# Kernel optimization log

Measured on AMD Instinct MI355X. Metric: run time of the kernel, lower is better.

## Reference

```python
import jax, jax.numpy as jnp
from jax import lax
import numpy as np

B, T, D = 8, 512, 512
TS = 2 * T          # skip length = upsampled length
DI, DS, DTR, K, NL = 2 * D, 16, 32, 4, 2  # d_inner, d_state, dt_rank, d_conv, n_layers


def setup_inputs() -> dict:
    key = jax.random.key(0)
    ks = jax.random.split(key, 12)
    f = lambda k, s: jax.random.normal(k, s, dtype=jnp.float32)
    sc = 0.02
    A_log = jnp.log(jnp.arange(1, DS + 1, dtype=jnp.float32))  # S4D-real init
    A_log = jnp.tile(A_log[None, None, :], (NL, DI, 1))
    return {
        "x": f(ks[0], (B, T, D)),
        "skip": f(ks[1], (B, TS, D)),
        "up_w": f(ks[2], (D, D, K)) * sc,        # torch ConvTranspose1d weight (in,out,k)
        "up_b": jnp.zeros((D,), jnp.float32),
        "merge_w": f(ks[3], (D, 2 * D)) * sc,    # 1x1 conv (out,in)
        "merge_b": jnp.zeros((D,), jnp.float32),
        "ln_w": jnp.ones((D,), jnp.float32),
        "ln_b": jnp.zeros((D,), jnp.float32),
        "in_proj_w": f(ks[4], (NL, 2 * DI, D)) * sc,
        "conv_w": f(ks[5], (NL, DI, K)) * sc,    # depthwise causal conv
        "conv_b": jnp.zeros((NL, DI), jnp.float32),
        "x_proj_w": f(ks[6], (NL, DTR + 2 * DS, DI)) * sc,
        "dt_proj_w": f(ks[7], (NL, DI, DTR)) * sc,
        "dt_proj_b": f(ks[8], (NL, DI)) * 0.1,
        "A_log": A_log,
        "D_param": jnp.ones((NL, DI), jnp.float32),
        "out_proj_w": f(ks[9], (NL, D, DI)) * sc,
    }


def _mamba(u, iw, cw, cb, xw, dw, db, alog, dpar, ow):
    # u: (B,L,D) -> (B,L,D). Standard Mamba block (expand=2, d_state=16, d_conv=4).
    b, L, _ = u.shape
    di, ds, dtr = cw.shape[0], alog.shape[1], dw.shape[1]
    xz = jnp.einsum('bld,ed->ble', u, iw)          # (B,L,2*di)
    xi, z = jnp.split(xz, 2, axis=-1)
    # depthwise causal conv over time
    xc = lax.conv_general_dilated(xi.transpose(0, 2, 1), cw[:, None, :], (1,),
                                  [(K - 1, 0)], feature_group_count=di,
                                  dimension_numbers=('NCH', 'OIH', 'NCH')) + cb[:, None]
    xc = jax.nn.silu(xc).transpose(0, 2, 1)        # (B,L,di)
    xdbl = jnp.einsum('bld,ed->ble', xc, xw)       # (B,L,dtr+2*ds)
    dt, Bm, Cm = jnp.split(xdbl, [dtr, dtr + ds], axis=-1)
    dt = jax.nn.softplus(jnp.einsum('blr,dr->bld', dt, dw) + db)  # (B,L,di)
    A = -jnp.exp(alog)                              # (di,ds)

    def step(h, inp):
        dt_t, B_t, C_t, u_t = inp                   # (B,di),(B,ds),(B,ds),(B,di)
        h = jnp.exp(dt_t[:, :, None] * A) * h + (dt_t * u_t)[:, :, None] * B_t[:, None, :]
        return h, jnp.einsum('bds,bs->bd', h, C_t)

    h0 = jnp.zeros((b, di, ds), u.dtype)
    _, ys = lax.scan(step, h0, (dt.transpose(1, 0, 2), Bm.transpose(1, 0, 2),
                                Cm.transpose(1, 0, 2), xc.transpose(1, 0, 2)))
    y = ys.transpose(1, 0, 2) + dpar * xc           # D skip connection
    y = y * jax.nn.silu(z)                          # gating
    return jnp.einsum('bld,od->blo', y, ow)


def reference(x, skip, up_w, up_b, merge_w, merge_b, ln_w, ln_b,
              in_proj_w, conv_w, conv_b, x_proj_w, dt_proj_w, dt_proj_b,
              A_log, D_param, out_proj_w):
    # ConvTranspose1d(k=4,s=2,p=1): dilated conv with flipped, transposed kernel
    kern = jnp.flip(jnp.swapaxes(up_w, 0, 1), -1)   # (out,in,k)
    xu = lax.conv_general_dilated(x.transpose(0, 2, 1), kern, (1,), [(2, 2)],
                                  lhs_dilation=(2,),
                                  dimension_numbers=('NCH', 'OIH', 'NCH')) + up_b[:, None]
    Ts = skip.shape[1]
    xu = xu[:, :, :Ts]                              # T_up == T_skip here (2T)
    cat = jnp.concatenate([xu.transpose(0, 2, 1), skip], axis=-1)  # (B,Ts,2D)
    merged = jnp.einsum('btc,oc->bto', cat, merge_w) + merge_b     # 1x1 conv merge
    mu = merged.mean(-1, keepdims=True)
    var = merged.var(-1, keepdims=True)
    out = (merged - mu) * lax.rsqrt(var + 1e-5) * ln_w + ln_b      # LayerNorm
    for i in range(in_proj_w.shape[0]):             # stacked Mamba layers
        out = _mamba(out, in_proj_w[i], conv_w[i], conv_b[i], x_proj_w[i],
                     dt_proj_w[i], dt_proj_b[i], A_log[i], D_param[i], out_proj_w[i])
    return out
```

## Files before the change

### kernel.cpp

```cpp
#include <hip/hip_runtime.h>

#define DEV __device__ __forceinline__

typedef short  bf16x8 __attribute__((ext_vector_type(8)));
typedef float  f32x4  __attribute__((ext_vector_type(4)));

DEV unsigned short f2b(float f) {
    unsigned int u = __float_as_uint(f);
    u += 0x7fffu + ((u >> 16) & 1u);
    return (unsigned short)(u >> 16);
}
DEV float b2f(unsigned short h) { return __uint_as_float((unsigned int)h << 16); }
DEV float silu(float x) { return x / (1.f + __expf(-x)); }
DEV float fexp2(float x) { return __builtin_amdgcn_exp2f(x); }
DEV float flog2(float x) { return __builtin_amdgcn_logf(x); }

typedef const __attribute__((address_space(1))) unsigned int GU32;
typedef __attribute__((address_space(3))) unsigned int LU32;
DEV void gload16(const unsigned short* g, unsigned short* l) {
    __builtin_amdgcn_global_load_lds((GU32*)g, (LU32*)l, 16, 0, 0);
}

__global__ __launch_bounds__(256) void k_cvt(const float* __restrict__ s,
                                             unsigned short* __restrict__ d, int n) {
    int i = (blockIdx.x * 256 + threadIdx.x) * 4;
    if (i + 3 < n) {
        float4 v = *(const float4*)(s + i);
        ushort4 o;
        o.x = f2b(v.x); o.y = f2b(v.y); o.z = f2b(v.z); o.w = f2b(v.w);
        *(ushort4*)(d + i) = o;
    }
}

__global__ void k_upT(const float* __restrict__ up_w, unsigned short* __restrict__ upT) {
    __shared__ float t[32][33];
    int tx = threadIdx.x, ty = threadIdx.y;
    int o0 = blockIdx.x * 32, i0 = blockIdx.y * 32, kz = blockIdx.z;
    t[ty][tx] = up_w[(size_t)(i0 + ty) * 2048 + (o0 + tx) * 4 + kz];
    __syncthreads();
    upT[(size_t)(kz * 512 + o0 + ty) * 512 + i0 + tx] = f2b(t[tx][ty]);
}

__global__ __launch_bounds__(256) void k_dtpackA(const float* __restrict__ xdbl,
                                                 unsigned short* __restrict__ Ap) {
    int i = blockIdx.x * 256 + threadIdx.x;
    int m = i >> 5, r = i & 31;
    float x = xdbl[(size_t)m * 64 + r];
    unsigned short xh = f2b(x);
    unsigned short xl = f2b(x - b2f(xh));
    size_t base = (size_t)m * 128;
    Ap[base + r]      = xh;
    Ap[base + 32 + r] = xl;
    Ap[base + 64 + r] = xh;
    Ap[base + 96 + r] = xl;
}

__global__ __launch_bounds__(256) void k_dtpackB(const float* __restrict__ w,
                                                 unsigned short* __restrict__ Bp) {
    int i = blockIdx.x * 256 + threadIdx.x;
    int d = i >> 5, r = i & 31;
    float x = w[(size_t)d * 32 + r];
    unsigned short wh = f2b(x);
    unsigned short wl = f2b(x - b2f(wh));
    size_t base = (size_t)d * 128;
    Bp[base + r]      = wh;
    Bp[base + 32 + r] = wl;
    Bp[base + 64 + r] = wl;
    Bp[base + 96 + r] = wh;
}

template <int BN, int OUTMODE>
__global__ __launch_bounds__(256) void k_gemm(const unsigned short* __restrict__ A,
                                              const unsigned short* __restrict__ B,
                                              float* __restrict__ Cf,
                                              unsigned short* __restrict__ Cb,
                                              const float* __restrict__ bias,
                                              int M, int N, int K) {
    constexpr int BM = 128, BK = 32;
    constexpr int WM = (BN == 128) ? 64 : 32;
    constexpr int WN = 64;
    constexpr int MI = WM / 16, NI = WN / 16;
    __shared__ unsigned short As[BM * BK];
    __shared__ unsigned short Bs[BN * BK];
    const int tid = threadIdx.x;
    const int wid = tid >> 6, lane = tid & 63;
    const int m0 = blockIdx.y * BM, n0 = blockIdx.x * BN;
    int wr, wc;
    if (BN == 128) { wr = wid >> 1; wc = wid & 1; } else { wr = wid; wc = 0; }
    const int wm0 = wr * WM, wn0 = wc * WN;
    const int fr = lane & 15, fh = lane >> 4;

    const int srow = wid * 16 + (lane >> 2);
    const int scol = (lane & 3) * 8;
    const unsigned short* Ag = A + (size_t)(m0 + srow) * K + scol;
    const unsigned short* Bg = B + (size_t)(n0 + srow) * K + scol;
    unsigned short* AsB = &As[wid * 16 * BK];
    unsigned short* BsB = &Bs[wid * 16 * BK];

    f32x4 acc[MI][NI];
#pragma unroll
    for (int i = 0; i < MI; ++i)
#pragma unroll
        for (int j = 0; j < NI; ++j) acc[i][j] = (f32x4){0.f, 0.f, 0.f, 0.f};

    for (int k0 = 0; k0 < K; k0 += BK) {
        gload16(Ag + k0, AsB);
        gload16(Ag + (size_t)64 * K + k0, AsB + 64 * BK);
        gload16(Bg + k0, BsB);
        if (BN == 128) gload16(Bg + (size_t)64 * K + k0, BsB + 64 * BK);
        __syncthreads();
        bf16x8 av[MI], bv[NI];
#pragma unroll
        for (int mi = 0; mi < MI; ++mi)
            av[mi] = *(const bf16x8*)(&As[(wm0 + mi * 16 + fr) * BK + fh * 8]);
#pragma unroll
        for (int ni = 0; ni < NI; ++ni)
            bv[ni] = *(const bf16x8*)(&Bs[(wn0 + ni * 16 + fr) * BK + fh * 8]);
#pragma unroll
        for (int mi = 0; mi < MI; ++mi)
#pragma unroll
            for (int ni = 0; ni < NI; ++ni)
                acc[mi][ni] = __builtin_amdgcn_mfma_f32_16x16x32_bf16(av[mi], bv[ni],
                                                                      acc[mi][ni], 0, 0, 0);
        __syncthreads();
    }
    constexpr float LOG2E = 1.4426950408889634f;
    constexpr float LN2   = 0.6931471805599453f;
#pragma unroll
    for (int mi = 0; mi < MI; ++mi) {
#pragma unroll
        for (int ni = 0; ni < NI; ++ni) {
            int col = n0 + wn0 + ni * 16 + fr;
            float bb = bias ? bias[col] : 0.f;
#pragma unroll
            for (int j = 0; j < 4; ++j) {
                int row = m0 + wm0 + mi * 16 + fh * 4 + j;
                float v = acc[mi][ni][j] + bb;
                if (OUTMODE == 0)      Cf[(size_t)row * N + col] = v;
                else if (OUTMODE == 1) Cb[(size_t)row * N + col] = f2b(v);
                else                   Cf[(size_t)row * N + col] =
                    (v > 20.f) ? v : flog2(1.f + fexp2(v * LOG2E)) * LN2;
            }
        }
    }
}

__global__ __launch_bounds__(256) void k_assemble(const float* __restrict__ P,
                                                  const float* __restrict__ skip,
                                                  const float* __restrict__ up_b,
                                                  unsigned short* __restrict__ catbf) {
    int bx = blockIdx.x;
    int m = bx >> 2;
    int c = (bx & 3) * 256 + threadIdx.x;
    int b = m >> 10, t = m & 1023, j = t >> 1;
    float v;
    if (c < 512) {
        size_t rb = (size_t)((b << 9) + j) * 2048;
        if (t & 1) {
            v = P[rb + 1024 + c];
            if (j + 1 < 512) v += P[rb + 2048 + c];
        } else {
            v = P[rb + 512 + c];
            if (j >= 1) v += P[rb - 2048 + 1536 + c];
        }
        v += up_b[c];
    } else {
        v = skip[(size_t)m * 512 + (c - 512)];
    }
    catbf[(size_t)m * 1024 + c] = f2b(v);
}

__global__ __launch_bounds__(256) void k_ln(const float* __restrict__ merged,
                                            const float* __restrict__ w,
                                            const float* __restrict__ bvec,
                                            unsigned short* __restrict__ outb) {
    int row = blockIdx.x * 4 + (threadIdx.x >> 6);
    int lane = threadIdx.x & 63;
    const float* r = merged + (size_t)row * 512 + lane * 8;
    float4 v1 = *(const float4*)r;
    float4 v2 = *(const float4*)(r + 4);
    float xv[8] = {v1.x, v1.y, v1.z, v1.w, v2.x, v2.y, v2.z, v2.w};
    float s = 0.f, ss = 0.f;
#pragma unroll
    for (int e = 0; e < 8; ++e) { s += xv[e]; ss += xv[e] * xv[e]; }
#pragma unroll
    for (int m = 1; m < 64; m <<= 1) { s += __shfl_xor(s, m, 64); ss += __shfl_xor(ss, m, 64); }
    float mean = s * (1.f / 512.f);
    float var = ss * (1.f / 512.f) - mean * mean;
    float inv = rsqrtf(var + 1e-5f);
    unsigned short o8[8];
#pragma unroll
    for (int e = 0; e < 8; ++e) {
        int c = lane * 8 + e;
        o8[e] = f2b((xv[e] - mean) * inv * w[c] + bvec[c]);
    }
    *(int4*)(outb + (size_t)row * 512 + lane * 8) = *(const int4*)o8;
}

__global__ __launch_bounds__(256) void k_conv(const unsigned short* __restrict__ xzb,
                                              const float* __restrict__ cw,
                                              const float* __restrict__ cb,
                                              float* __restrict__ xc,
                                              unsigned short* __restrict__ xcb) {
    int i = blockIdx.x * 256 + threadIdx.x;
    int m = i >> 8;
    int c0 = (i & 255) * 4;
    int l = m & 1023;
    float4 w0 = *(const float4*)(cw + (size_t)(c0 + 0) * 4);
    float4 w1 = *(const float4*)(cw + (size_t)(c0 + 1) * 4);
    float4 w2 = *(const float4*)(cw + (size_t)(c0 + 2) * 4);
    float4 w3 = *(const float4*)(cw + (size_t)(c0 + 3) * 4);
    float4 acc = *(const float4*)(cb + c0);
    const float* wp0 = (const float*)&w0;
    const float* wp1 = (const float*)&w1;
    const float* wp2 = (const float*)&w2;
    const float* wp3 = (const float*)&w3;
#pragma unroll
    for (int k = 0; k < 4; ++k) {
        int lp = l - 3 + k;
        if (lp >= 0) {
            ushort4 xv = *(const ushort4*)(xzb + (size_t)(m - l + lp) * 2048 + c0);
            acc.x = fmaf(wp0[k], b2f(xv.x), acc.x);
            acc.y = fmaf(wp1[k], b2f(xv.y), acc.y);
            acc.z = fmaf(wp2[k], b2f(xv.z), acc.z);
            acc.w = fmaf(wp3[k], b2f(xv.w), acc.w);
        }
    }
    float4 sv = { silu(acc.x), silu(acc.y), silu(acc.z), silu(acc.w) };
    *(float4*)(xc + (size_t)m * 1024 + c0) = sv;
    ushort4 o = { f2b(sv.x), f2b(sv.y), f2b(sv.z), f2b(sv.w) };
    *(ushort4*)(xcb + (size_t)m * 1024 + c0) = o;
}

constexpr int SCAN_NC = 32;
constexpr int SCAN_CL = 32;

template <int PHASE>
__global__ __launch_bounds__(256) void k_scan_chunk(
        const float* __restrict__ dt, const float* __restrict__ xc,
        const float* __restrict__ xdbl, const unsigned short* __restrict__ xzb,
        const float* __restrict__ Alog, const float* __restrict__ Dp,
        float* __restrict__ ap, float* __restrict__ hf,
        unsigned short* __restrict__ ybf) {
    constexpr int CL = SCAN_CL;
    const int d = blockIdx.x * 256 + threadIdx.x;
    const int b = blockIdx.y, c = blockIdx.z;
    const size_t mbase = (size_t)b * 1024 + (size_t)c * CL;

    __shared__ float sBC[CL][32];
    {
        int row = threadIdx.x >> 3, q = threadIdx.x & 7;
        *(float4*)&sBC[row][q * 4] =
            *(const float4*)(xdbl + (mbase + row) * 64 + 32 + q * 4);
    }
    __syncthreads();

    constexpr float LOG2E = 1.4426950408889634f;
    float A2[16], h[16];
#pragma unroll
    for (int s = 0; s < 16; ++s) A2[s] = -expf(Alog[d * 16 + s]) * LOG2E;

    bool powok = true;
#pragma unroll
    for (int s = 1; s < 16; ++s)
        powok = powok && (fabsf(A2[s] - (float)(s + 1) * A2[0]) <=
                          1e-5f * fabsf(A2[s]));

    const size_t sumbase = ((size_t)(b * SCAN_NC + c) << 14) + d * 16;
    if (PHASE == 0) {
#pragma unroll
        for (int s = 0; s < 16; ++s) h[s] = 0.f;
    } else {
#pragma unroll
        for (int s = 0; s < 16; s += 4)
            *(f32x4*)&h[s] = *(const f32x4*)(hf + sumbase + s);
    }
    float dtsum = 0.f;
    const float Dv = (PHASE == 1) ? Dp[d] : 0.f;

    const size_t mrow = mbase * 1024 + d;
    float dtv = dt[mrow], uv = xc[mrow];
#pragma unroll 2
    for (int l = 0; l < CL; ++l) {
        const size_t m = mbase + l;
        const float dtv_c = dtv, uv_c = uv;
        if (l + 1 < CL) {
            dtv = dt[mrow + (size_t)(l + 1) * 1024];
            uv  = xc[mrow + (size_t)(l + 1) * 1024];
        }
        float zv;
        if (PHASE == 1) zv = b2f(xzb[m * 2048 + 1024 + d]);
        const float dtu = dtv_c * uv_c;
        if (PHASE == 0) dtsum += dtv_c;
        float Bv[16], Cv[16];
#pragma unroll
        for (int q = 0; q < 4; ++q) {
            *(float4*)&Bv[q * 4] = *(const float4*)&sBC[l][q * 4];
            if (PHASE == 1)
                *(float4*)&Cv[q * 4] = *(const float4*)&sBC[l][16 + q * 4];
        }
        float p = 0.f;
        if (powok) {
            const float a1 = fexp2(dtv_c * A2[0]);
            float a = a1;
#pragma unroll
            for (int s = 0; s < 16; ++s) {
                h[s] = fmaf(a, h[s], dtu * Bv[s]);
                if (PHASE == 1) p = fmaf(h[s], Cv[s], p);
                a *= a1;
            }
        } else {
#pragma unroll
            for (int s = 0; s < 16; ++s) {
                float a = fexp2(dtv_c * A2[s]);
                h[s] = fmaf(a, h[s], dtu * Bv[s]);
                if (PHASE == 1) p = fmaf(h[s], Cv[s], p);
            }
        }
        if (PHASE == 1) {
            ybf[m * 1024 + d] = f2b((p + Dv * uv_c) * silu(zv));
        }
    }
    if (PHASE == 0) {
        float aprod[16];
        if (powok) {
            const float ap1 = fexp2(A2[0] * dtsum);
            float a = ap1;
#pragma unroll
            for (int s = 0; s < 16; ++s) { aprod[s] = a; a *= ap1; }
        } else {
#pragma unroll
            for (int s = 0; s < 16; ++s) aprod[s] = fexp2(A2[s] * dtsum);
        }
#pragma unroll
        for (int s = 0; s < 16; s += 4) {
            *(f32x4*)(ap + sumbase + s) = *(const f32x4*)&aprod[s];
            *(f32x4*)(hf + sumbase + s) = *(const f32x4*)&h[s];
        }
    }
}

__global__ __launch_bounds__(256) void k_scan_carry(const float* __restrict__ ap,
                                                    float* __restrict__ hf) {
    int i = blockIdx.x * 256 + threadIdx.x;
    int b = i >> 14, ds = i & 16383;
    float h = 0.f;
    for (int c = 0; c < SCAN_NC; ++c) {
        size_t idx = ((size_t)(b * SCAN_NC + c) << 14) + ds;
        float a = ap[idx], f = hf[idx];
        hf[idx] = h;
        h = fmaf(a, h, f);
    }
}

extern "C" void kernel_launch(void* const* d_in, const int* in_sizes, int n_in,
                              void* d_out, int out_size, void* d_ws, size_t ws_size,
                              hipStream_t stream) {
    const float* x         = (const float*)d_in[0];
    const float* skip      = (const float*)d_in[1];
    const float* up_w      = (const float*)d_in[2];
    const float* up_b      = (const float*)d_in[3];
    const float* merge_w   = (const float*)d_in[4];
    const float* merge_b   = (const float*)d_in[5];
    const float* ln_w      = (const float*)d_in[6];
    const float* ln_b      = (const float*)d_in[7];
    const float* in_proj_w = (const float*)d_in[8];
    const float* conv_w    = (const float*)d_in[9];
    const float* conv_b    = (const float*)d_in[10];
    const float* x_proj_w  = (const float*)d_in[11];
    const float* dt_proj_w = (const float*)d_in[12];
    const float* dt_proj_b = (const float*)d_in[13];
    const float* A_log     = (const float*)d_in[14];
    const float* D_param   = (const float*)d_in[15];
    const float* out_proj_w= (const float*)d_in[16];
    float* out = (float*)d_out;

    char* ws = (char*)d_ws;
    size_t off = 0;
    auto alloc = [&](size_t bytes) { size_t r = off; off += (bytes + 255) & ~(size_t)255; return r; };

    unsigned short* upT  = (unsigned short*)(ws + alloc(2048ull * 512 * 2));
    unsigned short* mw   = (unsigned short*)(ws + alloc(512ull * 1024 * 2));
    unsigned short* ipw  = (unsigned short*)(ws + alloc(2ull * 2048 * 512 * 2));
    unsigned short* xpw  = (unsigned short*)(ws + alloc(2ull * 64 * 1024 * 2));
    unsigned short* opw  = (unsigned short*)(ws + alloc(2ull * 512 * 1024 * 2));
    unsigned short* xbf  = (unsigned short*)(ws + alloc(4096ull * 512 * 2));
    unsigned short* ubf  = (unsigned short*)(ws + alloc(8192ull * 512 * 2));
    unsigned short* xzbf  = (unsigned short*)(ws + alloc(8192ull * 2048 * 2));
    float*          xc    = (float*)(ws + alloc(8192ull * 1024 * 4));
    unsigned short* xcbf  = (unsigned short*)(ws + alloc(8192ull * 1024 * 2));
    float*          xdbl  = (float*)(ws + alloc(8192ull * 64 * 4));
    float*          dtbuf = (float*)(ws + alloc(8192ull * 1024 * 4));
    unsigned short* ybf   = (unsigned short*)(ws + alloc(8192ull * 1024 * 2));
    float*          scan_ap = (float*)(ws + alloc((size_t)SCAN_NC * 8 * 16384 * 4));
    float*          scan_hf = (float*)(ws + alloc((size_t)SCAN_NC * 8 * 16384 * 4));
    unsigned short* dtpA  = (unsigned short*)(ws + alloc(8192ull * 128 * 2));
    unsigned short* dtpB  = (unsigned short*)(ws + alloc(1024ull * 128 * 2));
    float*          P      = (float*)xzbf;
    unsigned short* catbf  = (unsigned short*)xc;
    float*          merged = (float*)xcbf;

    k_cvt<<<2048, 256, 0, stream>>>(x, xbf, 4096 * 512);
    k_cvt<<<512, 256, 0, stream>>>(merge_w, mw, 512 * 1024);
    k_cvt<<<2048, 256, 0, stream>>>(in_proj_w, ipw, 2 * 2048 * 512);
    k_cvt<<<128, 256, 0, stream>>>(x_proj_w, xpw, 2 * 64 * 1024);
    k_cvt<<<1024, 256, 0, stream>>>(out_proj_w, opw, 2 * 512 * 1024);
    k_upT<<<dim3(16, 16, 4), dim3(32, 32), 0, stream>>>(up_w, upT);

    k_gemm<128, 0><<<dim3(16, 32), 256, 0, stream>>>(xbf, upT, P, nullptr, nullptr,
                                                     4096, 2048, 512);
    k_assemble<<<32768, 256, 0, stream>>>(P, skip, up_b, catbf);
    k_gemm<128, 0><<<dim3(4, 64), 256, 0, stream>>>(catbf, mw, merged, nullptr, merge_b,
                                                    8192, 512, 1024);
    k_ln<<<2048, 256, 0, stream>>>(merged, ln_w, ln_b, ubf);

    for (int li = 0; li < 2; ++li) {
        k_gemm<128, 1><<<dim3(16, 64), 256, 0, stream>>>(ubf, ipw + (size_t)li * 2048 * 512,
                                                         nullptr, xzbf, nullptr, 8192, 2048, 512);
        k_conv<<<8192, 256, 0, stream>>>(xzbf, conv_w + li * 4096, conv_b + li * 1024, xc, xcbf);
        k_gemm<64, 0><<<dim3(1, 64), 256, 0, stream>>>(xcbf, xpw + (size_t)li * 64 * 1024,
                                                       xdbl, nullptr, nullptr, 8192, 64, 1024);
        k_dtpackA<<<1024, 256, 0, stream>>>(xdbl, dtpA);
        k_dtpackB<<<128, 256, 0, stream>>>(dt_proj_w + (size_t)li * 32768, dtpB);
        k_gemm<64, 2><<<dim3(16, 64), 256, 0, stream>>>(dtpA, dtpB, dtbuf, nullptr,
                                                        dt_proj_b + (size_t)li * 1024,
                                                        8192, 1024, 128);
        const float* Al = A_log + (size_t)li * 1024 * 16;
        const float* Dl = D_param + (size_t)li * 1024;
        k_scan_chunk<0><<<dim3(4, 8, SCAN_NC), 256, 0, stream>>>(
            dtbuf, xc, xdbl, xzbf, Al, Dl, scan_ap, scan_hf, ybf);
        k_scan_carry<<<512, 256, 0, stream>>>(scan_ap, scan_hf);
        k_scan_chunk<1><<<dim3(4, 8, SCAN_NC), 256, 0, stream>>>(
            dtbuf, xc, xdbl, xzbf, Al, Dl, scan_ap, scan_hf, ybf);
        if (li == 0)
            k_gemm<128, 1><<<dim3(4, 64), 256, 0, stream>>>(ybf, opw, nullptr, ubf, nullptr,
                                                            8192, 512, 1024);
        else
            k_gemm<128, 0><<<dim3(4, 64), 256, 0, stream>>>(ybf, opw + (size_t)512 * 1024,
                                                            out, nullptr, nullptr, 8192, 512, 1024);
    }
}
```

Before: 481.1 us.

## Remap GEMM workgroups across XCDs and drop fp32 conv output buffer

The GEMM kernel now remaps its linear block id so that consecutive tiles land on the same XCD (chunked round-robin over 8 groups), aiming for better L2 reuse of shared A/B tiles. Separately, the depthwise conv no longer writes an fp32 copy of its activations; the scan reads the bf16 copy instead, removing a 32MB write plus the corresponding fp32 reads per layer. The cat buffer is re-aliased onto dtbuf. This trades some precision in the scan input (bf16 rounding of u) for less memory traffic.

```diff
diff --git a/kernel.cpp b/kernel.cpp
--- a/kernel.cpp
+++ b/kernel.cpp
@@ -84,7 +84,16 @@
     __shared__ unsigned short Bs[BN * BK];
     const int tid = threadIdx.x;
     const int wid = tid >> 6, lane = tid & 63;
-    const int m0 = blockIdx.y * BM, n0 = blockIdx.x * BN;
+
+    int bid = blockIdx.y * gridDim.x + blockIdx.x;
+    const int nwg = gridDim.x * gridDim.y;
+    if ((nwg & 7) == 0) {
+        int cpx = nwg >> 3;
+        bid = (bid & 7) * cpx + (bid >> 3);
+    }
+    const int bx = bid % gridDim.x, by = bid / gridDim.x;
+    const int m0 = by * BM, n0 = bx * BN;
+
     int wr, wc;
     if (BN == 128) { wr = wid >> 1; wc = wid & 1; } else { wr = wid; wc = 0; }
     const int wm0 = wr * WM, wn0 = wc * WN;
@@ -200,7 +209,6 @@
 __global__ __launch_bounds__(256) void k_conv(const unsigned short* __restrict__ xzb,
                                               const float* __restrict__ cw,
                                               const float* __restrict__ cb,
-                                              float* __restrict__ xc,
                                               unsigned short* __restrict__ xcb) {
     int i = blockIdx.x * 256 + threadIdx.x;
     int m = i >> 8;
@@ -226,9 +234,7 @@
             acc.w = fmaf(wp3[k], b2f(xv.w), acc.w);
         }
     }
-    float4 sv = { silu(acc.x), silu(acc.y), silu(acc.z), silu(acc.w) };
-    *(float4*)(xc + (size_t)m * 1024 + c0) = sv;
-    ushort4 o = { f2b(sv.x), f2b(sv.y), f2b(sv.z), f2b(sv.w) };
+    ushort4 o = { f2b(silu(acc.x)), f2b(silu(acc.y)), f2b(silu(acc.z)), f2b(silu(acc.w)) };
     *(ushort4*)(xcb + (size_t)m * 1024 + c0) = o;
 }
 
@@ -237,7 +243,7 @@
 
 template <int PHASE>
 __global__ __launch_bounds__(256) void k_scan_chunk(
-        const float* __restrict__ dt, const float* __restrict__ xc,
+        const float* __restrict__ dt, const unsigned short* __restrict__ xcb,
         const float* __restrict__ xdbl, const unsigned short* __restrict__ xzb,
         const float* __restrict__ Alog, const float* __restrict__ Dp,
         float* __restrict__ ap, float* __restrict__ hf,
@@ -279,14 +285,15 @@
     const float Dv = (PHASE == 1) ? Dp[d] : 0.f;
 
     const size_t mrow = mbase * 1024 + d;
-    float dtv = dt[mrow], uv = xc[mrow];
+    float dtv = dt[mrow];
+    float uv  = b2f(xcb[mrow]);
 #pragma unroll 2
     for (int l = 0; l < CL; ++l) {
         const size_t m = mbase + l;
         const float dtv_c = dtv, uv_c = uv;
         if (l + 1 < CL) {
             dtv = dt[mrow + (size_t)(l + 1) * 1024];
-            uv  = xc[mrow + (size_t)(l + 1) * 1024];
+            uv  = b2f(xcb[mrow + (size_t)(l + 1) * 1024]);
         }
         float zv;
         if (PHASE == 1) zv = b2f(xzb[m * 2048 + 1024 + d]);
@@ -387,7 +394,6 @@
     unsigned short* xbf  = (unsigned short*)(ws + alloc(4096ull * 512 * 2));
     unsigned short* ubf  = (unsigned short*)(ws + alloc(8192ull * 512 * 2));
     unsigned short* xzbf  = (unsigned short*)(ws + alloc(8192ull * 2048 * 2));
-    float*          xc    = (float*)(ws + alloc(8192ull * 1024 * 4));
     unsigned short* xcbf  = (unsigned short*)(ws + alloc(8192ull * 1024 * 2));
     float*          xdbl  = (float*)(ws + alloc(8192ull * 64 * 4));
     float*          dtbuf = (float*)(ws + alloc(8192ull * 1024 * 4));
@@ -397,7 +403,7 @@
     unsigned short* dtpA  = (unsigned short*)(ws + alloc(8192ull * 128 * 2));
     unsigned short* dtpB  = (unsigned short*)(ws + alloc(1024ull * 128 * 2));
     float*          P      = (float*)xzbf;
-    unsigned short* catbf  = (unsigned short*)xc;
+    unsigned short* catbf  = (unsigned short*)dtbuf;
     float*          merged = (float*)xcbf;
 
     k_cvt<<<2048, 256, 0, stream>>>(x, xbf, 4096 * 512);
@@ -417,7 +423,7 @@
     for (int li = 0; li < 2; ++li) {
         k_gemm<128, 1><<<dim3(16, 64), 256, 0, stream>>>(ubf, ipw + (size_t)li * 2048 * 512,
                                                          nullptr, xzbf, nullptr, 8192, 2048, 512);
-        k_conv<<<8192, 256, 0, stream>>>(xzbf, conv_w + li * 4096, conv_b + li * 1024, xc, xcbf);
+        k_conv<<<8192, 256, 0, stream>>>(xzbf, conv_w + li * 4096, conv_b + li * 1024, xcbf);
         k_gemm<64, 0><<<dim3(1, 64), 256, 0, stream>>>(xcbf, xpw + (size_t)li * 64 * 1024,
                                                        xdbl, nullptr, nullptr, 8192, 64, 1024);
         k_dtpackA<<<1024, 256, 0, stream>>>(xdbl, dtpA);
@@ -428,10 +434,10 @@
         const float* Al = A_log + (size_t)li * 1024 * 16;
         const float* Dl = D_param + (size_t)li * 1024;
         k_scan_chunk<0><<<dim3(4, 8, SCAN_NC), 256, 0, stream>>>(
-            dtbuf, xc, xdbl, xzbf, Al, Dl, scan_ap, scan_hf, ybf);
+            dtbuf, xcbf, xdbl, xzbf, Al, Dl, scan_ap, scan_hf, ybf);
         k_scan_carry<<<512, 256, 0, stream>>>(scan_ap, scan_hf);
         k_scan_chunk<1><<<dim3(4, 8, SCAN_NC), 256, 0, stream>>>(
-            dtbuf, xc, xdbl, xzbf, Al, Dl, scan_ap, scan_hf, ybf);
+            dtbuf, xcbf, xdbl, xzbf, Al, Dl, scan_ap, scan_hf, ybf);
         if (li == 0)
             k_gemm<128, 1><<<dim3(4, 64), 256, 0, stream>>>(ybf, opw, nullptr, ubf, nullptr,
                                                             8192, 512, 1024);
```

After: 468.4 us. 1.03x faster.
